# Kernel tuning notes

Measured on AMD Instinct MI355X. Metric: run time of the kernel, lower is better.

Reference implementation:

```python
import jax, jax.numpy as jnp
import numpy as np


def _adder2d(x, w, stride, padding):
    """AdderNet 'convolution': out[b,o,i,j] = -sum_p |patch[b,p,i,j] - w[o,p]|.

    x: [B, C, H, W], w: [O, C, kh, kw]. Patches are extracted in (C, kh, kw)
    channel-major order, matching torch.nn.functional.unfold / w.reshape(O, -1).
    """
    O, C, kh, kw = w.shape
    patches = jax.lax.conv_general_dilated_patches(
        x, (kh, kw), (stride, stride), [(padding, padding), (padding, padding)])
    B, P, Ho, Wo = patches.shape  # P = C*kh*kw
    p = patches.reshape(B, P, Ho * Wo)
    wf = w.reshape(O, P)

    def per_out(wo):  # sequential over small O to avoid a [B,O,P,L] blowup
        return -jnp.sum(jnp.abs(p - wo[None, :, None]), axis=1)  # [B, L]

    out = jax.lax.map(per_out, wf)  # [O, B, L]
    return jnp.transpose(out, (1, 0, 2)).reshape(B, O, Ho, Wo)


def setup_inputs() -> dict:
    key = jax.random.key(0)
    ks = jax.random.split(key, 5)
    x = jax.random.normal(ks[0], (4096, 1, 28, 28), dtype=jnp.float32)
    w1 = jax.random.normal(ks[1], (16, 1, 3, 3), dtype=jnp.float32)
    w2 = jax.random.normal(ks[2], (32, 16, 3, 3), dtype=jnp.float32)
    w3 = jax.random.normal(ks[3], (16, 32, 3, 3), dtype=jnp.float32)
    w4 = jax.random.normal(ks[4], (10, 16, 3, 3), dtype=jnp.float32)
    return {"x": x, "w1": w1, "w2": w2, "w3": w3, "w4": w4}


def reference(x, w1, w2, w3, w4):
    h = x - 0.5
    h = jax.nn.relu((_adder2d(h, w1, 2, 0) + 10.0) / 4.0)   # [B,16,13,13]
    h = jax.nn.relu((_adder2d(h, w2, 2, 1) + 130.0) / 8.0)  # [B,32,7,7]
    h = jax.nn.relu((_adder2d(h, w3, 2, 1) + 280.0) / 16.0)  # [B,16,4,4]
    h = _adder2d(h, w4, 2, 0)                                # [B,10,1,1]
    h = h.reshape(h.shape[0], -1)                            # [B,10]
    return jax.nn.log_softmax(h, axis=1)
```

## Files before the change

kernel.cpp:

```cpp
#include <hip/hip_runtime.h>
#include <math.h>


#if defined(__has_builtin)
#if __has_builtin(__builtin_amdgcn_sad_u16)
#define HAS_SAD 1
#endif
#endif

__device__ __forceinline__ unsigned sadu16(unsigned a, unsigned b, unsigned acc) {
#ifdef HAS_SAD
  return __builtin_amdgcn_sad_u16(a, b, acc);
#else
  int al = (int)(a & 0xFFFFu), ah = (int)(a >> 16);
  int bl = (int)(b & 0xFFFFu), bh = (int)(b >> 16);
  return acc + (unsigned)(al > bl ? al - bl : bl - al)
             + (unsigned)(ah > bh ? ah - bh : bh - ah);
#endif
}

__device__ __forceinline__ unsigned quant(float v) {
  return (unsigned)fmaf(v, 1024.0f, 8192.5f);
}
__device__ __forceinline__ unsigned quantx(float v) {
  return (unsigned)fmaf(v, 1024.0f, 7680.5f);
}
__device__ __forceinline__ int imax(int a, int b) { return a > b ? a : b; }

#define QPAD 0x20002000u

__global__ void adder_prep(const float* __restrict__ w1, const float* __restrict__ w2,
                           const float* __restrict__ w3, const float* __restrict__ w4,
                           unsigned* __restrict__ qw) {
  int k = blockIdx.x * 256 + threadIdx.x;
  if (k < 96) {
    int o = k / 6, r = k % 6, kh = r >> 1, h = r & 1;
    const float* p = w1 + o * 9 + kh * 3;
    qw[k] = h ? quant(p[2]) : (quant(p[0]) | (quant(p[1]) << 16));
  } else if (k < 2400) {
    int k2 = k - 96, m = k2 / 288, r = k2 % 288, o = r / 9, pk = r % 9;
    int s = o * 144 + 2 * m * 9 + pk;
    qw[k] = quant(w2[s]) | (quant(w2[s + 9]) << 16);
  } else if (k < 4704) {
    int k3 = k - 2400, m2 = k3 / 144, r = k3 % 144, o = r / 9, pk = r % 9;
    int s = o * 288 + 2 * m2 * 9 + pk;
    qw[k] = quant(w3[s]) | (quant(w3[s + 9]) << 16);
  } else if (k < 5424) {
    int k4 = k - 4704, m = k4 / 90, r = k4 % 90, o = r / 9, pk = r % 9;
    int s = o * 144 + 2 * m * 9 + pk;
    qw[k] = quant(w4[s]) | (quant(w4[s + 9]) << 16);
  }
}

__global__ __launch_bounds__(64, 3) void adder_main(
    const float* __restrict__ gx,
    const unsigned* __restrict__ qw,
    float* __restrict__ gout)
{
  __shared__ __align__(16) unsigned sA1[1800];
  __shared__ __align__(16) unsigned sA2[1296];

  const int t = threadIdx.x;
  const int b = blockIdx.x;
  const float* img = gx + (size_t)b * 784;

  for (int k = t; k < 448; k += 64) {
    int plane = k / 56, c = k % 56;
    int y, x;
    if (c < 15)      { y = 0;      x = c; }
    else if (c < 30) { y = 14;     x = c - 15; }
    else if (c < 43) { y = c - 29; x = 0; }
    else             { y = c - 42; x = 14; }
    sA1[plane * 225 + y * 15 + x] = QPAD;
  }
  for (int k = t; k < 512; k += 64) {
    int plane = k >> 5, c = k & 31;
    int y, x;
    if (c < 9)       { y = 0; x = c; }
    else if (c < 18) { y = 8; x = c - 9; }
    else if (c < 25) { y = c - 17; x = 0; }
    else             { y = c - 24; x = 8; }
    sA2[plane * 81 + y * 9 + x] = QPAD;
  }

  if (t < 52) {
    const int i = t >> 2, jq = t & 3;
    unsigned r[3][5], mw[3][4];
#pragma unroll
    for (int kh = 0; kh < 3; ++kh) {
      const float* rp = img + (2 * i + kh) * 28 + 8 * jq;
      float4 A = *(const float4*)(rp);
      float4 B = *(const float4*)(rp + 4);
      float2 C = *(const float2*)(rp + 8);
      r[kh][0] = quantx(A.x) | (quantx(A.y) << 16);
      r[kh][1] = quantx(A.z) | (quantx(A.w) << 16);
      r[kh][2] = quantx(B.x) | (quantx(B.y) << 16);
      r[kh][3] = quantx(B.z) | (quantx(B.w) << 16);
      r[kh][4] = quantx(C.x) | (quantx(C.y) << 16);
#pragma unroll
      for (int c = 0; c < 4; ++c) mw[kh][c] = r[kh][c + 1] & 0xFFFFu;
    }
#pragma unroll 1
    for (int op = 0; op < 8; ++op) {
      const unsigned* w = qw + op * 12;
      unsigned a0[4], a1[4];
#pragma unroll
      for (int jj = 0; jj < 4; ++jj) { a0[jj] = 0u; a1[jj] = 0u; }
#pragma unroll
      for (int kh = 0; kh < 3; ++kh) {
        unsigned wa01 = w[kh * 2], wa2 = w[kh * 2 + 1];
        unsigned wb01 = w[6 + kh * 2], wb2 = w[6 + kh * 2 + 1];
#pragma unroll
        for (int jj = 0; jj < 4; ++jj) {
          a0[jj] = sadu16(r[kh][jj], wa01, a0[jj]);
          a0[jj] = sadu16(mw[kh][jj], wa2, a0[jj]);
          a1[jj] = sadu16(r[kh][jj], wb01, a1[jj]);
          a1[jj] = sadu16(mw[kh][jj], wb2, a1[jj]);
        }
      }
      unsigned* dst = sA1 + op * 225 + (i + 1) * 15 + 4 * jq + 1;
#pragma unroll
      for (int jj = 0; jj < 4; ++jj) {
        if (4 * jq + jj < 13) {
          int q0 = imax(10752 - (int)((a0[jj] + 2u) >> 2), 8192);
          int q1 = imax(10752 - (int)((a1[jj] + 2u) >> 2), 8192);
          dst[jj] = (unsigned)q0 | ((unsigned)q1 << 16);
        }
      }
    }
  }
  __syncthreads();

  if (t < 49) {
    const int i = t / 7, j = t % 7;
    unsigned acc[32];
#pragma unroll
    for (int o = 0; o < 32; ++o) acc[o] = 0u;
    const unsigned* qw2 = qw + 96;
#pragma unroll 1
    for (int m = 0; m < 8; ++m) {
      const unsigned* plane = sA1 + m * 225 + 2 * j;
      unsigned p[3][3];
#pragma unroll
      for (int kh = 0; kh < 3; ++kh)
#pragma unroll
        for (int c = 0; c < 3; ++c)
          p[kh][c] = plane[(2 * i + kh) * 15 + c];
      const unsigned* wm = qw2 + m * 288;
#pragma unroll
      for (int o = 0; o < 32; ++o) {
        const unsigned* w9 = wm + o * 9;
        unsigned a = acc[o];
#pragma unroll
        for (int kh = 0; kh < 3; ++kh)
#pragma unroll
          for (int c = 0; c < 3; ++c)
            a = sadu16(p[kh][c], w9[kh * 3 + c], a);
        acc[o] = a;
      }
    }
#pragma unroll
    for (int m2 = 0; m2 < 16; ++m2) {
      int q0 = imax(24832 - (int)((acc[2 * m2] + 4u) >> 3), 8192);
      int q1 = imax(24832 - (int)((acc[2 * m2 + 1] + 4u) >> 3), 8192);
      sA2[m2 * 81 + (i + 1) * 9 + (j + 1)] = (unsigned)q0 | ((unsigned)q1 << 16);
    }
  }
  __syncthreads();

  {
    const int pos = t & 15, og = (t >> 4) & 1, mg = t >> 5;
    const int i = pos >> 2, j = pos & 3;
    unsigned acc[8];
#pragma unroll
    for (int o = 0; o < 8; ++o) acc[o] = 0u;
    const unsigned* qw3 = qw + 2400;
#pragma unroll 1
    for (int mm = 0; mm < 8; ++mm) {
      const int m2 = mg * 8 + mm;
      const unsigned* plane = sA2 + m2 * 81 + 2 * j;
      unsigned p[3][3];
#pragma unroll
      for (int kh = 0; kh < 3; ++kh)
#pragma unroll
        for (int c = 0; c < 3; ++c)
          p[kh][c] = plane[(2 * i + kh) * 9 + c];
      const unsigned* ws = qw3 + m2 * 144 + og * 72;
#pragma unroll
      for (int oo = 0; oo < 8; ++oo) {
        const unsigned* w9 = ws + oo * 9;
        unsigned a = acc[oo];
#pragma unroll
        for (int kh = 0; kh < 3; ++kh)
#pragma unroll
          for (int c = 0; c < 3; ++c)
            a = sadu16(p[kh][c], w9[kh * 3 + c], a);
        acc[oo] = a;
      }
    }
    unsigned* pp = sA1 + t * 12;
    *(uint4*)(pp)     = make_uint4(acc[0], acc[1], acc[2], acc[3]);
    *(uint4*)(pp + 4) = make_uint4(acc[4], acc[5], acc[6], acc[7]);
  }
  __syncthreads();

  if (t < 16) {
    const int pos = t;
#pragma unroll
    for (int m = 0; m < 8; ++m) {
      const int og = m >> 2, oo = 2 * (m & 3);
      const int b0 = (og * 16 + pos) * 12;
      unsigned s0 = sA1[b0 + oo]     + sA1[b0 + 384 + oo];
      unsigned s1 = sA1[b0 + oo + 1] + sA1[b0 + 384 + oo + 1];
      int q0 = imax(26112 - (int)((s0 + 8u) >> 4), 8192);
      int q1 = imax(26112 - (int)((s1 + 8u) >> 4), 8192);
      sA1[800 + m * 17 + pos] = (unsigned)q0 | ((unsigned)q1 << 16);
    }
  }
  __syncthreads();

  if (t < 40) {
    const int o = t % 10, mq = t / 10;
    const unsigned* qw4 = qw + 4704;
    unsigned acc = 0u;
#pragma unroll
    for (int mm = 0; mm < 2; ++mm) {
      const int m = mq * 2 + mm;
      const unsigned* a3 = sA1 + 800 + m * 17;
      const unsigned* w9 = qw4 + (m * 10 + o) * 9;
#pragma unroll
      for (int kh = 0; kh < 3; ++kh)
#pragma unroll
        for (int kw = 0; kw < 3; ++kw)
          acc = sadu16(a3[kh * 4 + kw], w9[kh * 3 + kw], acc);
    }
    sA1[940 + t] = acc;
  }
  __syncthreads();
  if (t < 10) {
    unsigned s = sA1[940 + t] + sA1[950 + t] + sA1[960 + t] + sA1[970 + t];
    ((float*)sA1)[980 + t] = -(float)s * (1.0f / 1024.0f);
  }
  __syncthreads();
  if (t < 10) {
    const float* lg = (const float*)sA1 + 980;
    float mx = lg[0];
#pragma unroll
    for (int k = 1; k < 10; ++k) mx = fmaxf(mx, lg[k]);
    float sum = 0.0f;
#pragma unroll
    for (int k = 0; k < 10; ++k) sum += __expf(lg[k] - mx);
    gout[(size_t)b * 10 + t] = lg[t] - mx - __logf(sum);
  }
}

extern "C" void kernel_launch(void* const* d_in, const int* in_sizes, int n_in,
                              void* d_out, int out_size, void* d_ws, size_t ws_size,
                              hipStream_t stream) {
  const float* x  = (const float*)d_in[0];
  const float* w1 = (const float*)d_in[1];
  const float* w2 = (const float*)d_in[2];
  const float* w3 = (const float*)d_in[3];
  const float* w4 = (const float*)d_in[4];
  unsigned* qw = (unsigned*)d_ws;
  float* out = (float*)d_out;
  adder_prep<<<22, 256, 0, stream>>>(w1, w2, w3, w4, qw);
  adder_main<<<4096, 64, 0, stream>>>(x, qw, out);
}
```

Before: 117.8 us.

## Drop padded LDS halos, mask borders in registers, raise occupancy bound

Stores the intermediate activation planes unpadded (13x13 and 7x7 instead of 15x15 and 9x9), so the per-block halo-fill loops go away. Border taps are now handled by clamped offsets plus a select that substitutes the pad value. The smaller LDS footprint allows launch_bounds to ask for 4 blocks per SIMD, and the channel loops are unrolled by 2. The cost is extra per-tap selects and the risk of higher register pressure under the tighter bound.

```diff
diff --git a/kernel.cpp b/kernel.cpp
--- a/kernel.cpp
+++ b/kernel.cpp
@@ -52,36 +52,17 @@
   }
 }
 
-__global__ __launch_bounds__(64, 3) void adder_main(
+__global__ __launch_bounds__(64, 4) void adder_main(
     const float* __restrict__ gx,
     const unsigned* __restrict__ qw,
     float* __restrict__ gout)
 {
-  __shared__ __align__(16) unsigned sA1[1800];
-  __shared__ __align__(16) unsigned sA2[1296];
+  __shared__ __align__(16) unsigned sA1[1352];
+  __shared__ __align__(16) unsigned sA2[784];
 
   const int t = threadIdx.x;
   const int b = blockIdx.x;
   const float* img = gx + (size_t)b * 784;
-
-  for (int k = t; k < 448; k += 64) {
-    int plane = k / 56, c = k % 56;
-    int y, x;
-    if (c < 15)      { y = 0;      x = c; }
-    else if (c < 30) { y = 14;     x = c - 15; }
-    else if (c < 43) { y = c - 29; x = 0; }
-    else             { y = c - 42; x = 14; }
-    sA1[plane * 225 + y * 15 + x] = QPAD;
-  }
-  for (int k = t; k < 512; k += 64) {
-    int plane = k >> 5, c = k & 31;
-    int y, x;
-    if (c < 9)       { y = 0; x = c; }
-    else if (c < 18) { y = 8; x = c - 9; }
-    else if (c < 25) { y = c - 17; x = 0; }
-    else             { y = c - 24; x = 8; }
-    sA2[plane * 81 + y * 9 + x] = QPAD;
-  }
 
   if (t < 52) {
     const int i = t >> 2, jq = t & 3;
@@ -118,7 +99,7 @@
           a1[jj] = sadu16(mw[kh][jj], wb2, a1[jj]);
         }
       }
-      unsigned* dst = sA1 + op * 225 + (i + 1) * 15 + 4 * jq + 1;
+      unsigned* dst = sA1 + op * 169 + i * 13 + 4 * jq;
 #pragma unroll
       for (int jj = 0; jj < 4; ++jj) {
         if (4 * jq + jj < 13) {
@@ -133,19 +114,32 @@
 
   if (t < 49) {
     const int i = t / 7, j = t % 7;
+    int ro[3], co[3];
+    bool rv[3], cv[3];
+#pragma unroll
+    for (int k = 0; k < 3; ++k) {
+      int r = 2 * i - 1 + k;
+      rv[k] = (r >= 0) && (r < 13);
+      ro[k] = rv[k] ? r * 13 : 0;
+      int c = 2 * j - 1 + k;
+      cv[k] = (c >= 0) && (c < 13);
+      co[k] = cv[k] ? c : 0;
+    }
     unsigned acc[32];
 #pragma unroll
     for (int o = 0; o < 32; ++o) acc[o] = 0u;
     const unsigned* qw2 = qw + 96;
-#pragma unroll 1
+#pragma unroll 2
     for (int m = 0; m < 8; ++m) {
-      const unsigned* plane = sA1 + m * 225 + 2 * j;
+      const unsigned* plane = sA1 + m * 169;
       unsigned p[3][3];
 #pragma unroll
       for (int kh = 0; kh < 3; ++kh)
 #pragma unroll
-        for (int c = 0; c < 3; ++c)
-          p[kh][c] = plane[(2 * i + kh) * 15 + c];
+        for (int c = 0; c < 3; ++c) {
+          unsigned v = plane[ro[kh] + co[c]];
+          p[kh][c] = (rv[kh] && cv[c]) ? v : QPAD;
+        }
       const unsigned* wm = qw2 + m * 288;
 #pragma unroll
       for (int o = 0; o < 32; ++o) {
@@ -163,7 +157,7 @@
     for (int m2 = 0; m2 < 16; ++m2) {
       int q0 = imax(24832 - (int)((acc[2 * m2] + 4u) >> 3), 8192);
       int q1 = imax(24832 - (int)((acc[2 * m2 + 1] + 4u) >> 3), 8192);
-      sA2[m2 * 81 + (i + 1) * 9 + (j + 1)] = (unsigned)q0 | ((unsigned)q1 << 16);
+      sA2[m2 * 49 + i * 7 + j] = (unsigned)q0 | ((unsigned)q1 << 16);
     }
   }
   __syncthreads();
@@ -171,20 +165,33 @@
   {
     const int pos = t & 15, og = (t >> 4) & 1, mg = t >> 5;
     const int i = pos >> 2, j = pos & 3;
+    int ro[3], co[3];
+    bool rv[3], cv[3];
+#pragma unroll
+    for (int k = 0; k < 3; ++k) {
+      int r = 2 * i - 1 + k;
+      rv[k] = (r >= 0) && (r < 7);
+      ro[k] = rv[k] ? r * 7 : 0;
+      int c = 2 * j - 1 + k;
+      cv[k] = (c >= 0) && (c < 7);
+      co[k] = cv[k] ? c : 0;
+    }
     unsigned acc[8];
 #pragma unroll
     for (int o = 0; o < 8; ++o) acc[o] = 0u;
     const unsigned* qw3 = qw + 2400;
-#pragma unroll 1
+#pragma unroll 2
     for (int mm = 0; mm < 8; ++mm) {
       const int m2 = mg * 8 + mm;
-      const unsigned* plane = sA2 + m2 * 81 + 2 * j;
+      const unsigned* plane = sA2 + m2 * 49;
       unsigned p[3][3];
 #pragma unroll
       for (int kh = 0; kh < 3; ++kh)
 #pragma unroll
-        for (int c = 0; c < 3; ++c)
-          p[kh][c] = plane[(2 * i + kh) * 9 + c];
+        for (int c = 0; c < 3; ++c) {
+          unsigned v = plane[ro[kh] + co[c]];
+          p[kh][c] = (rv[kh] && cv[c]) ? v : QPAD;
+        }
       const unsigned* ws = qw3 + m2 * 144 + og * 72;
 #pragma unroll
       for (int oo = 0; oo < 8; ++oo) {
```

Result: slower. 127.9 us (+8.5%).
